# Kernel optimization log

Hardware: AMD Instinct MI355X
Metric: run time of the kernel (lower is better)

The kernel has to match this reference:

```python
import jax, jax.numpy as jnp
import numpy as np

JOINT_CHAINS = {'wrist': ['WRJ1', 'WRJ2'], 'index': ['FFJ4', 'FFJ3', 'FFJ2', 'FFJ1'], 'middle': ['MFJ4', 'MFJ3', 'MFJ2', 'MFJ1'], 'ring': ['RFJ4', 'RFJ3', 'RFJ2', 'RFJ1'], 'little': ['LFJ5', 'LFJ4', 'LFJ3', 'LFJ2', 'LFJ1'], 'thumb': ['THJ5', 'THJ4', 'THJ3', 'THJ2', 'THJ1']}
JOINT_NAMES = ['WRJ1', 'WRJ2', 'FFJ4', 'FFJ3', 'FFJ2', 'FFJ1', 'MFJ4', 'MFJ3', 'MFJ2', 'MFJ1', 'RFJ4', 'RFJ3', 'RFJ2', 'RFJ1', 'LFJ5', 'LFJ4', 'LFJ3', 'LFJ2', 'LFJ1', 'THJ5', 'THJ4', 'THJ3', 'THJ2', 'THJ1']
N_JOINTS = 24


def _build_a_norm():
    # Fixed 24-node kinematic-chain graph, undirected, with self loops,
    # symmetric degree normalization (PyG GCNConv default).
    idx = {n: i for i, n in enumerate(JOINT_NAMES)}
    A = np.zeros((N_JOINTS, N_JOINTS), dtype=np.float32)
    for chain in JOINT_CHAINS.values():
        for i in range(len(chain) - 1):
            u, v = idx[chain[i]], idx[chain[i + 1]]
            A[u, v] = 1.0
            A[v, u] = 1.0
    A = A + np.eye(N_JOINTS, dtype=np.float32)  # add self loops
    deg = A.sum(axis=1)
    dinv = 1.0 / np.sqrt(deg)
    return (dinv[:, None] * A * dinv[None, :]).astype(np.float32)


def setup_inputs() -> dict:
    key = jax.random.key(0)
    k1, k2, k3, k4, k5 = jax.random.split(key, 5)
    B, N, Cin, H, O = 8192, N_JOINTS, 64, 256, 256
    return {
        'node_feats': jax.random.normal(k1, (B, N, Cin), dtype=jnp.float32),
        'W1': jax.random.normal(k2, (Cin, H), dtype=jnp.float32) * 0.05,
        'b1': jax.random.normal(k3, (H,), dtype=jnp.float32) * 0.05,
        'W2': jax.random.normal(k4, (H, O), dtype=jnp.float32) * 0.05,
        'b2': jax.random.normal(k5, (O,), dtype=jnp.float32) * 0.05,
        'A_norm': jnp.asarray(_build_a_norm()),
    }


def reference(node_feats, W1, b1, W2, b2, A_norm):
    # GCNConv layer 1: linear then degree-normalized aggregation, then ReLU
    h = jnp.einsum('nm,bmh->bnh', A_norm, node_feats @ W1) + b1  # (B, N, H)
    h = jax.nn.relu(h)
    # GCNConv layer 2
    h = jnp.einsum('nm,bmo->bno', A_norm, h @ W2) + b2  # (B, N, O)
    h = jax.nn.relu(h)
    # global mean pool over the N=24 nodes of each graph
    return h.mean(axis=1)  # (B, O)
```

## Files before the change

kernel.cpp:

```cpp
#include <hip/hip_runtime.h>
#include <stdint.h>


typedef __attribute__((ext_vector_type(8))) __bf16 bf16x8;
typedef __attribute__((ext_vector_type(4))) __bf16 bf16x4;
typedef __attribute__((ext_vector_type(4))) float f32x4;

#define SWZ(row, byteoff) ((unsigned)(byteoff) ^ ((((unsigned)(row)) & 7u) << 4))

__global__ void prep_kernel(const float* __restrict__ W1,
                            const float* __restrict__ W2,
                            unsigned char* __restrict__ ws) {
  int t = blockIdx.x * blockDim.x + threadIdx.x;
  bf16x8 v;
  if (t < 2048) {
    int blk = t >> 6, l = t & 63;
    int ks = blk & 1, hf = blk >> 1;
    int h  = hf * 16 + (l & 15);
    int k0 = ks * 32 + (l >> 4) * 8;
#pragma unroll
    for (int j = 0; j < 8; ++j) v[j] = (__bf16)W1[(k0 + j) * 256 + h];
    *(bf16x8*)(ws + t * 16) = v;
  } else if (t < 10240) {
    int t2 = t - 2048;
    int blk = t2 >> 6, l = t2 & 63;
    int ks = blk & 1;
    int c  = (blk >> 1) & 3;
    int of = blk >> 3;
    int o  = of * 16 + (l & 15);
    int f0 = c * 64 + ks * 32 + (l >> 4) * 8;
#pragma unroll
    for (int j = 0; j < 8; ++j) v[j] = (__bf16)W2[(f0 + j) * 256 + o];
    *(bf16x8*)(ws + 32768 + t2 * 16) = v;
  }
}

__launch_bounds__(256, 2)
__global__ void gnn_kernel(const float* __restrict__ X,
                           const float* __restrict__ b1g,
                           const float* __restrict__ b2g,
                           const float* __restrict__ Ag,
                           const unsigned char* __restrict__ ws,
                           float* __restrict__ out) {
  __shared__ __align__(16) unsigned char buf[96 * 512];
  __shared__ __align__(16) float ldsB1[256];
  __shared__ __align__(16) float ldsB2[256];

  const int tid  = threadIdx.x;
  const int lane = tid & 63;
  const int wid  = tid >> 6;
  const int g0   = blockIdx.x * 4;
  const long row0 = (long)g0 * 24;

  ldsB1[tid] = b1g[tid];
  ldsB2[tid] = b2g[tid];

  const int r16   = lane & 15;
  const int kgrp  = (lane >> 4) * 8;
  const int lbyte = lane * 16;

  bf16x8 af1[2][4];
#pragma unroll
  for (int ks = 0; ks < 2; ++ks)
#pragma unroll
    for (int fi = 0; fi < 4; ++fi)
      af1[ks][fi] = *(const bf16x8*)(ws + ((((wid * 4 + fi) * 2) + ks) << 10) + lbyte);

#pragma unroll
  for (int it = 0; it < 6; ++it) {
    int idx = tid + it * 256;
    int m   = idx >> 4;
    int c4  = (idx & 15) * 4;
    int n   = m - (m / 24) * 24;
    const float* xr = X + (row0 + m) * 64 + c4;
    float wmid = Ag[n * 25];
    float wdn  = (n > 0)  ? Ag[n * 25 - 1] : 0.f;
    float wup  = (n < 23) ? Ag[n * 25 + 1] : 0.f;
    float4 xc = *(const float4*)xr;
    float ax = wmid * xc.x, ay = wmid * xc.y, az = wmid * xc.z, aw = wmid * xc.w;
    if (wdn != 0.f) {
      float4 xd = *(const float4*)(xr - 64);
      ax += wdn * xd.x; ay += wdn * xd.y; az += wdn * xd.z; aw += wdn * xd.w;
    }
    if (wup != 0.f) {
      float4 xu = *(const float4*)(xr + 64);
      ax += wup * xu.x; ay += wup * xu.y; az += wup * xu.z; aw += wup * xu.w;
    }
    bf16x4 p;
    p[0] = (__bf16)ax; p[1] = (__bf16)ay; p[2] = (__bf16)az; p[3] = (__bf16)aw;
    *(bf16x4*)(buf + SWZ(m, m * 128 + c4 * 2)) = p;
  }
  __syncthreads();

  f32x4 acc[4][6];
  const f32x4 z4 = {0.f, 0.f, 0.f, 0.f};
#pragma unroll
  for (int i = 0; i < 4; ++i)
#pragma unroll
    for (int j = 0; j < 6; ++j) acc[i][j] = z4;

#pragma unroll
  for (int ks = 0; ks < 2; ++ks) {
    bf16x8 bf[6];
    int koff = (ks * 32 + kgrp) * 2;
#pragma unroll
    for (int fj = 0; fj < 6; ++fj) {
      int m = fj * 16 + r16;
      bf[fj] = *(const bf16x8*)(buf + SWZ(m, m * 128 + koff));
    }
    __builtin_amdgcn_s_setprio(1);
#pragma unroll
    for (int fi = 0; fi < 4; ++fi)
#pragma unroll
      for (int fj = 0; fj < 6; ++fj)
        acc[fi][fj] = __builtin_amdgcn_mfma_f32_16x16x32_bf16(af1[ks][fi], bf[fj], acc[fi][fj], 0, 0, 0);
    __builtin_amdgcn_s_setprio(0);
  }
  __syncthreads();

  {
    int hr = (lane >> 4) * 4;
#pragma unroll
    for (int fi = 0; fi < 4; ++fi) {
      int h = wid * 64 + fi * 16 + hr;
      float4 bb = *(const float4*)&ldsB1[h];
#pragma unroll
      for (int fj = 0; fj < 6; ++fj) {
        int m = fj * 16 + r16;
        f32x4 v = acc[fi][fj];
        bf16x4 p;
        p[0] = (__bf16)fmaxf(v[0] + bb.x, 0.f);
        p[1] = (__bf16)fmaxf(v[1] + bb.y, 0.f);
        p[2] = (__bf16)fmaxf(v[2] + bb.z, 0.f);
        p[3] = (__bf16)fmaxf(v[3] + bb.w, 0.f);
        *(bf16x4*)(buf + SWZ(m, m * 512 + h * 2)) = p;
      }
    }
  }
  __syncthreads();

#pragma unroll
  for (int i = 0; i < 4; ++i)
#pragma unroll
    for (int j = 0; j < 6; ++j) acc[i][j] = z4;

  const unsigned char* w2p = ws + 32768;
#pragma unroll
  for (int c = 0; c < 4; ++c) {
#pragma unroll
    for (int ks = 0; ks < 2; ++ks) {
      bf16x8 af[4], bf[6];
      int foff = (c * 64 + ks * 32 + kgrp) * 2;
#pragma unroll
      for (int fi = 0; fi < 4; ++fi)
        af[fi] = *(const bf16x8*)(w2p + (((((wid * 4 + fi) * 4) + c) * 2 + ks) << 10) + lbyte);
#pragma unroll
      for (int fj = 0; fj < 6; ++fj) {
        int m = fj * 16 + r16;
        bf[fj] = *(const bf16x8*)(buf + SWZ(m, m * 512 + foff));
      }
      __builtin_amdgcn_s_setprio(1);
#pragma unroll
      for (int fi = 0; fi < 4; ++fi)
#pragma unroll
        for (int fj = 0; fj < 6; ++fj)
          acc[fi][fj] = __builtin_amdgcn_mfma_f32_16x16x32_bf16(af[fi], bf[fj], acc[fi][fj], 0, 0, 0);
      __builtin_amdgcn_s_setprio(0);
    }
  }
  __syncthreads();

  {
    int orr = (lane >> 4) * 4;
#pragma unroll
    for (int fi = 0; fi < 4; ++fi) {
      int o = wid * 64 + fi * 16 + orr;
#pragma unroll
      for (int fj = 0; fj < 6; ++fj) {
        int m = fj * 16 + r16;
        f32x4 v = acc[fi][fj];
        bf16x4 p;
        p[0] = (__bf16)v[0]; p[1] = (__bf16)v[1];
        p[2] = (__bf16)v[2]; p[3] = (__bf16)v[3];
        *(bf16x4*)(buf + SWZ(m, m * 512 + o * 2)) = p;
      }
    }
  }
  __syncthreads();

  {
    const int g  = wid;
    const int o4 = lane * 4;
    const int rb = g * 24;
    float4 bt = *(const float4*)&ldsB2[o4];
    float bb[4] = {bt.x, bt.y, bt.z, bt.w};
    float s[4]  = {0.f, 0.f, 0.f, 0.f};
    float zp[4] = {0.f, 0.f, 0.f, 0.f};
    float zc[4], zn[4];
    {
      bf16x4 z = *(const bf16x4*)(buf + SWZ(rb, rb * 512 + o4 * 2));
      bf16x4 y = *(const bf16x4*)(buf + SWZ(rb + 1, (rb + 1) * 512 + o4 * 2));
#pragma unroll
      for (int j = 0; j < 4; ++j) { zc[j] = (float)z[j]; zn[j] = (float)y[j]; }
    }
#pragma unroll
    for (int nn = 0; nn < 24; ++nn) {
      const float w0 = Ag[nn * 25];
      float q[4];
#pragma unroll
      for (int j = 0; j < 4; ++j) q[j] = w0 * zc[j] + bb[j];
      if (nn > 0) {
        const float wd = Ag[nn * 25 - 1];
#pragma unroll
        for (int j = 0; j < 4; ++j) q[j] += wd * zp[j];
      }
      if (nn < 23) {
        const float wu = Ag[nn * 25 + 1];
#pragma unroll
        for (int j = 0; j < 4; ++j) q[j] += wu * zn[j];
      }
#pragma unroll
      for (int j = 0; j < 4; ++j) s[j] += fmaxf(q[j], 0.f);
#pragma unroll
      for (int j = 0; j < 4; ++j) { zp[j] = zc[j]; zc[j] = zn[j]; }
      if (nn < 22) {
        int r = rb + nn + 2;
        bf16x4 z = *(const bf16x4*)(buf + SWZ(r, r * 512 + o4 * 2));
#pragma unroll
        for (int j = 0; j < 4; ++j) zn[j] = (float)z[j];
      }
    }
    float4 r4;
    r4.x = s[0] * (1.f / 24.f);
    r4.y = s[1] * (1.f / 24.f);
    r4.z = s[2] * (1.f / 24.f);
    r4.w = s[3] * (1.f / 24.f);
    *(float4*)(out + (size_t)(g0 + g) * 256 + o4) = r4;
  }
}

extern "C" void kernel_launch(void* const* d_in, const int* in_sizes, int n_in,
                              void* d_out, int out_size, void* d_ws, size_t ws_size,
                              hipStream_t stream) {
  (void)n_in; (void)out_size; (void)ws_size;
  const float* X  = (const float*)d_in[0];
  const float* W1 = (const float*)d_in[1];
  const float* b1 = (const float*)d_in[2];
  const float* W2 = (const float*)d_in[3];
  const float* b2 = (const float*)d_in[4];
  const float* A  = (const float*)d_in[5];
  float* out = (float*)d_out;
  unsigned char* ws = (unsigned char*)d_ws;

  int B = in_sizes[0] / (24 * 64);
  prep_kernel<<<40, 256, 0, stream>>>(W1, W2, ws);
  gnn_kernel<<<B / 4, 256, 0, stream>>>(X, b1, b2, A, ws, out);
}
```

Baseline: 63.97 us.

## Split GNN block across 8 waves over row halves with separate LDS buffers

After: 58.38 us. 1.1x faster.

```diff
diff --git a/kernel.cpp b/kernel.cpp
--- a/kernel.cpp
+++ b/kernel.cpp
@@ -4,6 +4,7 @@
 
 typedef __attribute__((ext_vector_type(8))) __bf16 bf16x8;
 typedef __attribute__((ext_vector_type(4))) __bf16 bf16x4;
+typedef __attribute__((ext_vector_type(2))) __bf16 bf16x2;
 typedef __attribute__((ext_vector_type(4))) float f32x4;
 
 #define SWZ(row, byteoff) ((unsigned)(byteoff) ^ ((((unsigned)(row)) & 7u) << 4))
@@ -35,40 +36,35 @@
   }
 }
 
-__launch_bounds__(256, 2)
+__launch_bounds__(512, 4)
 __global__ void gnn_kernel(const float* __restrict__ X,
                            const float* __restrict__ b1g,
                            const float* __restrict__ b2g,
                            const float* __restrict__ Ag,
                            const unsigned char* __restrict__ ws,
                            float* __restrict__ out) {
-  __shared__ __align__(16) unsigned char buf[96 * 512];
+  __shared__ __align__(16) unsigned char ldsX[96 * 128];
+  __shared__ __align__(16) unsigned char ldsH[96 * 512];
   __shared__ __align__(16) float ldsB1[256];
   __shared__ __align__(16) float ldsB2[256];
 
   const int tid  = threadIdx.x;
   const int lane = tid & 63;
   const int wid  = tid >> 6;
+  const int ow   = wid & 3;
+  const int mw   = wid >> 2;
   const int g0   = blockIdx.x * 4;
   const long row0 = (long)g0 * 24;
 
-  ldsB1[tid] = b1g[tid];
-  ldsB2[tid] = b2g[tid];
+  if (tid < 256) { ldsB1[tid] = b1g[tid]; ldsB2[tid] = b2g[tid]; }
 
   const int r16   = lane & 15;
   const int kgrp  = (lane >> 4) * 8;
   const int lbyte = lane * 16;
 
-  bf16x8 af1[2][4];
-#pragma unroll
-  for (int ks = 0; ks < 2; ++ks)
-#pragma unroll
-    for (int fi = 0; fi < 4; ++fi)
-      af1[ks][fi] = *(const bf16x8*)(ws + ((((wid * 4 + fi) * 2) + ks) << 10) + lbyte);
-
-#pragma unroll
-  for (int it = 0; it < 6; ++it) {
-    int idx = tid + it * 256;
+#pragma unroll
+  for (int it = 0; it < 3; ++it) {
+    int idx = tid + it * 512;
     int m   = idx >> 4;
     int c4  = (idx & 15) * 4;
     int n   = m - (m / 24) * 24;
@@ -88,52 +84,54 @@
     }
     bf16x4 p;
     p[0] = (__bf16)ax; p[1] = (__bf16)ay; p[2] = (__bf16)az; p[3] = (__bf16)aw;
-    *(bf16x4*)(buf + SWZ(m, m * 128 + c4 * 2)) = p;
-  }
-  __syncthreads();
-
-  f32x4 acc[4][6];
+    *(bf16x4*)(ldsX + SWZ(m, m * 128 + c4 * 2)) = p;
+  }
+  __syncthreads();
+
+  f32x4 acc[4][3];
   const f32x4 z4 = {0.f, 0.f, 0.f, 0.f};
 #pragma unroll
   for (int i = 0; i < 4; ++i)
 #pragma unroll
-    for (int j = 0; j < 6; ++j) acc[i][j] = z4;
+    for (int j = 0; j < 3; ++j) acc[i][j] = z4;
 
 #pragma unroll
   for (int ks = 0; ks < 2; ++ks) {
-    bf16x8 bf[6];
+    bf16x8 af[4], bf[3];
     int koff = (ks * 32 + kgrp) * 2;
 #pragma unroll
-    for (int fj = 0; fj < 6; ++fj) {
-      int m = fj * 16 + r16;
-      bf[fj] = *(const bf16x8*)(buf + SWZ(m, m * 128 + koff));
+    for (int fi = 0; fi < 4; ++fi)
+      af[fi] = *(const bf16x8*)(ws + ((((ow * 4 + fi) * 2) + ks) << 10) + lbyte);
+#pragma unroll
+    for (int fj = 0; fj < 3; ++fj) {
+      int m = mw * 48 + fj * 16 + r16;
+      bf[fj] = *(const bf16x8*)(ldsX + SWZ(m, m * 128 + koff));
     }
     __builtin_amdgcn_s_setprio(1);
 #pragma unroll
     for (int fi = 0; fi < 4; ++fi)
 #pragma unroll
-      for (int fj = 0; fj < 6; ++fj)
-        acc[fi][fj] = __builtin_amdgcn_mfma_f32_16x16x32_bf16(af1[ks][fi], bf[fj], acc[fi][fj], 0, 0, 0);
+      for (int fj = 0; fj < 3; ++fj)
+        acc[fi][fj] = __builtin_amdgcn_mfma_f32_16x16x32_bf16(af[fi], bf[fj], acc[fi][fj], 0, 0, 0);
     __builtin_amdgcn_s_setprio(0);
   }
-  __syncthreads();
 
   {
     int hr = (lane >> 4) * 4;
 #pragma unroll
     for (int fi = 0; fi < 4; ++fi) {
-      int h = wid * 64 + fi * 16 + hr;
+      int h = ow * 64 + fi * 16 + hr;
       float4 bb = *(const float4*)&ldsB1[h];
 #pragma unroll
-      for (int fj = 0; fj < 6; ++fj) {
-        int m = fj * 16 + r16;
+      for (int fj = 0; fj < 3; ++fj) {
+        int m = mw * 48 + fj * 16 + r16;
         f32x4 v = acc[fi][fj];
         bf16x4 p;
         p[0] = (__bf16)fmaxf(v[0] + bb.x, 0.f);
         p[1] = (__bf16)fmaxf(v[1] + bb.y, 0.f);
         p[2] = (__bf16)fmaxf(v[2] + bb.z, 0.f);
         p[3] = (__bf16)fmaxf(v[3] + bb.w, 0.f);
-        *(bf16x4*)(buf + SWZ(m, m * 512 + h * 2)) = p;
+        *(bf16x4*)(ldsH + SWZ(m, m * 512 + h * 2)) = p;
       }
     }
   }
@@ -142,31 +140,42 @@
 #pragma unroll
   for (int i = 0; i < 4; ++i)
 #pragma unroll
-    for (int j = 0; j < 6; ++j) acc[i][j] = z4;
+    for (int j = 0; j < 3; ++j) acc[i][j] = z4;
 
   const unsigned char* w2p = ws + 32768;
-#pragma unroll
-  for (int c = 0; c < 4; ++c) {
-#pragma unroll
-    for (int ks = 0; ks < 2; ++ks) {
-      bf16x8 af[4], bf[6];
-      int foff = (c * 64 + ks * 32 + kgrp) * 2;
+  bf16x8 afc[4];
+#pragma unroll
+  for (int fi = 0; fi < 4; ++fi)
+    afc[fi] = *(const bf16x8*)(w2p + ((((ow * 4 + fi) * 4 + 0) * 2 + 0) << 10) + lbyte);
+
+#pragma unroll
+  for (int s = 0; s < 8; ++s) {
+    const int c  = s >> 1;
+    const int ks = s & 1;
+    bf16x8 afn[4];
+    if (s < 7) {
+      const int c2  = (s + 1) >> 1;
+      const int ks2 = (s + 1) & 1;
 #pragma unroll
       for (int fi = 0; fi < 4; ++fi)
-        af[fi] = *(const bf16x8*)(w2p + (((((wid * 4 + fi) * 4) + c) * 2 + ks) << 10) + lbyte);
-#pragma unroll
-      for (int fj = 0; fj < 6; ++fj) {
-        int m = fj * 16 + r16;
-        bf[fj] = *(const bf16x8*)(buf + SWZ(m, m * 512 + foff));
-      }
-      __builtin_amdgcn_s_setprio(1);
-#pragma unroll
-      for (int fi = 0; fi < 4; ++fi)
-#pragma unroll
-        for (int fj = 0; fj < 6; ++fj)
-          acc[fi][fj] = __builtin_amdgcn_mfma_f32_16x16x32_bf16(af[fi], bf[fj], acc[fi][fj], 0, 0, 0);
-      __builtin_amdgcn_s_setprio(0);
-    }
+        afn[fi] = *(const bf16x8*)(w2p + ((((ow * 4 + fi) * 4 + c2) * 2 + ks2) << 10) + lbyte);
+    }
+    bf16x8 bf[3];
+    int foff = (c * 64 + ks * 32 + kgrp) * 2;
+#pragma unroll
+    for (int fj = 0; fj < 3; ++fj) {
+      int m = mw * 48 + fj * 16 + r16;
+      bf[fj] = *(const bf16x8*)(ldsH + SWZ(m, m * 512 + foff));
+    }
+    __builtin_amdgcn_s_setprio(1);
+#pragma unroll
+    for (int fi = 0; fi < 4; ++fi)
+#pragma unroll
+      for (int fj = 0; fj < 3; ++fj)
+        acc[fi][fj] = __builtin_amdgcn_mfma_f32_16x16x32_bf16(afc[fi], bf[fj], acc[fi][fj], 0, 0, 0);
+    __builtin_amdgcn_s_setprio(0);
+#pragma unroll
+    for (int fi = 0; fi < 4; ++fi) afc[fi] = afn[fi];
   }
   __syncthreads();
 
@@ -174,68 +183,64 @@
     int orr = (lane >> 4) * 4;
 #pragma unroll
     for (int fi = 0; fi < 4; ++fi) {
-      int o = wid * 64 + fi * 16 + orr;
-#pragma unroll
-      for (int fj = 0; fj < 6; ++fj) {
-        int m = fj * 16 + r16;
+      int o = ow * 64 + fi * 16 + orr;
+#pragma unroll
+      for (int fj = 0; fj < 3; ++fj) {
+        int m = mw * 48 + fj * 16 + r16;
         f32x4 v = acc[fi][fj];
         bf16x4 p;
         p[0] = (__bf16)v[0]; p[1] = (__bf16)v[1];
         p[2] = (__bf16)v[2]; p[3] = (__bf16)v[3];
-        *(bf16x4*)(buf + SWZ(m, m * 512 + o * 2)) = p;
+        *(bf16x4*)(ldsH + SWZ(m, m * 512 + o * 2)) = p;
       }
     }
   }
   __syncthreads();
 
   {
-    const int g  = wid;
-    const int o4 = lane * 4;
+    const int g  = wid & 3;
+    const int o2 = (wid >> 2) * 128 + lane * 2;
     const int rb = g * 24;
-    float4 bt = *(const float4*)&ldsB2[o4];
-    float bb[4] = {bt.x, bt.y, bt.z, bt.w};
-    float s[4]  = {0.f, 0.f, 0.f, 0.f};
-    float zp[4] = {0.f, 0.f, 0.f, 0.f};
-    float zc[4], zn[4];
+    float bb[2] = { ldsB2[o2], ldsB2[o2 + 1] };
+    float s[2]  = {0.f, 0.f};
+    float zp[2] = {0.f, 0.f};
+    float zc[2], zn[2];
     {
-      bf16x4 z = *(const bf16x4*)(buf + SWZ(rb, rb * 512 + o4 * 2));
-      bf16x4 y = *(const bf16x4*)(buf + SWZ(rb + 1, (rb + 1) * 512 + o4 * 2));
-#pragma unroll
-      for (int j = 0; j < 4; ++j) { zc[j] = (float)z[j]; zn[j] = (float)y[j]; }
+      bf16x2 z = *(const bf16x2*)(ldsH + SWZ(rb, rb * 512 + o2 * 2));
+      bf16x2 y = *(const bf16x2*)(ldsH + SWZ(rb + 1, (rb + 1) * 512 + o2 * 2));
+      zc[0] = (float)z[0]; zc[1] = (float)z[1];
+      zn[0] = (float)y[0]; zn[1] = (float)y[1];
     }
 #pragma unroll
     for (int nn = 0; nn < 24; ++nn) {
       const float w0 = Ag[nn * 25];
-      float q[4];
-#pragma unroll
-      for (int j = 0; j < 4; ++j) q[j] = w0 * zc[j] + bb[j];
+      float q[2];
+#pragma unroll
+      for (int j = 0; j < 2; ++j) q[j] = w0 * zc[j] + bb[j];
       if (nn > 0) {
         const float wd = Ag[nn * 25 - 1];
 #pragma unroll
-        for (int j = 0; j < 4; ++j) q[j] += wd * zp[j];
+        for (int j = 0; j < 2; ++j) q[j] += wd * zp[j];
       }
       if (nn < 23) {
         const float wu = Ag[nn * 25 + 1];
 #pragma unroll
-        for (int j = 0; j < 4; ++j) q[j] += wu * zn[j];
-      }
-#pragma unroll
-      for (int j = 0; j < 4; ++j) s[j] += fmaxf(q[j], 0.f);
-#pragma unroll
-      for (int j = 0; j < 4; ++j) { zp[j] = zc[j]; zc[j] = zn[j]; }
+        for (int j = 0; j < 2; ++j) q[j] += wu * zn[j];
+      }
+#pragma unroll
+      for (int j = 0; j < 2; ++j) s[j] += fmaxf(q[j], 0.f);
+#pragma unroll
+      for (int j = 0; j < 2; ++j) { zp[j] = zc[j]; zc[j] = zn[j]; }
       if (nn < 22) {
         int r = rb + nn + 2;
-        bf16x4 z = *(const bf16x4*)(buf + SWZ(r, r * 512 + o4 * 2));
-#pragma unroll
-        for (int j = 0; j < 4; ++j) zn[j] = (float)z[j];
-      }
-    }
-    float4 r4;
-    r4.x = s[0] * (1.f / 24.f);
-    r4.y = s[1] * (1.f / 24.f);
-    r4.z = s[2] * (1.f / 24.f);
-    r4.w = s[3] * (1.f / 24.f);
-    *(float4*)(out + (size_t)(g0 + g) * 256 + o4) = r4;
+        bf16x2 z = *(const bf16x2*)(ldsH + SWZ(r, r * 512 + o2 * 2));
+        zn[0] = (float)z[0]; zn[1] = (float)z[1];
+      }
+    }
+    float2 r2;
+    r2.x = s[0] * (1.f / 24.f);
+    r2.y = s[1] * (1.f / 24.f);
+    *(float2*)(out + (size_t)(g0 + g) * 256 + o2) = r2;
   }
 }
 
@@ -254,5 +259,5 @@
 
   int B = in_sizes[0] / (24 * 64);
   prep_kernel<<<40, 256, 0, stream>>>(W1, W2, ws);
-  gnn_kernel<<<B / 4, 256, 0, stream>>>(X, b1, b2, A, ws, out);
+  gnn_kernel<<<B / 4, 512, 0, stream>>>(X, b1, b2, A, ws, out);
 }
```
